# Performance work log

Measured on AMD Instinct MI355X. Metric: run time of the kernel, lower is better.

## Reference

```python
import jax, jax.numpy as jnp
import numpy as np

D_MODEL, N_HEADS, D_LLM = 1024, 16, 4096
D_KEYS = D_MODEL // N_HEADS  # 64


def setup_inputs() -> dict:
    key = jax.random.key(0)
    ks = jax.random.split(key, 11)
    s = lambda fan_in: 1.0 / np.sqrt(fan_in)
    inp = {
        "target_embedding": jax.random.normal(ks[0], (4, 2048, D_MODEL), jnp.float32),
        "source_embedding": jax.random.normal(ks[1], (4, 1024, D_LLM), jnp.float32),
        "value_embedding": jax.random.normal(ks[2], (4, 1024, D_LLM), jnp.float32),
        "Wq": jax.random.uniform(ks[3], (D_MODEL, D_KEYS * N_HEADS), jnp.float32, -s(D_MODEL), s(D_MODEL)),
        "bq": jax.random.uniform(ks[4], (D_KEYS * N_HEADS,), jnp.float32, -s(D_MODEL), s(D_MODEL)),
        "Wk": jax.random.uniform(ks[5], (D_LLM, D_KEYS * N_HEADS), jnp.float32, -s(D_LLM), s(D_LLM)),
        "bk": jax.random.uniform(ks[6], (D_KEYS * N_HEADS,), jnp.float32, -s(D_LLM), s(D_LLM)),
        "Wv": jax.random.uniform(ks[7], (D_LLM, D_KEYS * N_HEADS), jnp.float32, -s(D_LLM), s(D_LLM)),
        "bv": jax.random.uniform(ks[8], (D_KEYS * N_HEADS,), jnp.float32, -s(D_LLM), s(D_LLM)),
        "Wo": jax.random.uniform(ks[9], (D_KEYS * N_HEADS, D_MODEL), jnp.float32, -s(D_KEYS * N_HEADS), s(D_KEYS * N_HEADS)),
        "bo": jax.random.uniform(ks[10], (D_MODEL,), jnp.float32, -s(D_KEYS * N_HEADS), s(D_KEYS * N_HEADS)),
    }
    return inp


def reference(target_embedding, source_embedding, value_embedding,
              Wq, bq, Wk, bk, Wv, bv, Wo, bo):
    B, L, _ = target_embedding.shape
    _, S, _ = source_embedding.shape
    H, E = N_HEADS, D_KEYS
    q = (target_embedding @ Wq + bq).reshape(B, L, H, E)
    k = (source_embedding @ Wk + bk).reshape(B, S, H, E)
    v = (value_embedding @ Wv + bv).reshape(B, S, H, E)
    scale = 1.0 / np.sqrt(E)
    scores = jnp.einsum('blhe,bshe->bhls', q, k)  # [B,H,L,S]
    A = jax.nn.softmax(scale * scores, axis=-1)   # dropout = identity (eval mode)
    out = jnp.einsum('bhls,bshe->blhe', A, v).reshape(B, L, H * E)
    return out @ Wo + bo
```

## Files before the change

### kernel.cpp

```cpp
#include <hip/hip_runtime.h>
#include <hip/hip_bf16.h>

using bf16 = __hip_bfloat16;
typedef __attribute__((ext_vector_type(8))) short short8;
typedef __attribute__((ext_vector_type(4))) float f32x4;

static constexpr int Bc = 4, Lc = 2048, Sc = 1024;
static constexpr int DModel = 1024;

__device__ __forceinline__ void gload16(const void* g, void* l) {
  __builtin_amdgcn_global_load_lds((const __attribute__((address_space(1))) void*)g,
                                   (__attribute__((address_space(3))) void*)l,
                                   16, 0, 0);
}

__device__ __forceinline__ void wait_vm8()  { asm volatile("s_waitcnt vmcnt(8)" ::: "memory"); }
__device__ __forceinline__ void wait_vm6()  { asm volatile("s_waitcnt vmcnt(6)" ::: "memory"); }
__device__ __forceinline__ void wait_vm4()  { asm volatile("s_waitcnt vmcnt(4)" ::: "memory"); }
__device__ __forceinline__ void wait_vm3()  { asm volatile("s_waitcnt vmcnt(3)" ::: "memory"); }
__device__ __forceinline__ void wait_vm0()  { asm volatile("s_waitcnt vmcnt(0)" ::: "memory"); }
__device__ __forceinline__ void barrier_raw() { asm volatile("s_barrier" ::: "memory"); }

__global__ void cvt3(const float* __restrict__ a, bf16* __restrict__ ao, long na4,
                     const float* __restrict__ b, bf16* __restrict__ bo, long nb4,
                     const float* __restrict__ c, bf16* __restrict__ co, long nc4) {
  long total = na4 + nb4 + nc4;
  long stride = (long)gridDim.x * blockDim.x;
  for (long i = (long)blockIdx.x * blockDim.x + threadIdx.x; i < total; i += stride) {
    const float* src; bf16* dst; long j;
    if (i < na4)            { src = a; dst = ao; j = i; }
    else if (i < na4 + nb4) { src = b; dst = bo; j = i - na4; }
    else                    { src = c; dst = co; j = i - na4 - nb4; }
    float4 v = reinterpret_cast<const float4*>(src)[j];
    alignas(8) bf16 t[4] = {__float2bfloat16(v.x), __float2bfloat16(v.y),
                            __float2bfloat16(v.z), __float2bfloat16(v.w)};
    reinterpret_cast<ushort4*>(dst)[j] = *reinterpret_cast<const ushort4*>(t);
  }
}

__global__ __launch_bounds__(256) void transpose_cvt_w(const float* __restrict__ Wq, bf16* __restrict__ WqT,
                                                       const float* __restrict__ Wk, bf16* __restrict__ WkT,
                                                       const float* __restrict__ Wv, bf16* __restrict__ WvT,
                                                       const float* __restrict__ Wo, bf16* __restrict__ WoT) {
  __shared__ bf16 tile[32][33];
  int bid = blockIdx.x;
  const float* in; bf16* out; int R, l;
  if (bid < 1024)      { in = Wq; out = WqT; R = 1024; l = bid; }
  else if (bid < 5120) { in = Wk; out = WkT; R = 4096; l = bid - 1024; }
  else if (bid < 9216) { in = Wv; out = WvT; R = 4096; l = bid - 5120; }
  else                 { in = Wo; out = WoT; R = 1024; l = bid - 9216; }
  const int C = 1024;
  int bx = l & 31, by = l >> 5;
  int tx = threadIdx.x & 31, ty = threadIdx.x >> 5;
  int r0 = by * 32, c0 = bx * 32;
#pragma unroll
  for (int i = 0; i < 32; i += 8)
    tile[ty + i][tx] = __float2bfloat16(in[(long)(r0 + ty + i) * C + c0 + tx]);
  __syncthreads();
#pragma unroll
  for (int i = 0; i < 32; i += 8)
    out[(long)(c0 + ty + i) * R + r0 + tx] = tile[tx][ty + i];
}

__device__ __forceinline__ void gemm_bal_core(const bf16* __restrict__ A, const bf16* __restrict__ Bt,
                                              const float* __restrict__ bias,
                                              bf16* __restrict__ Cb, bf16* __restrict__ Cvt,
                                              int K, int bx, int by, bf16* lds) {
  const int tid = threadIdx.x;
  const int lane = tid & 63, g = lane >> 4, lm = lane & 15;
  const int wid = tid >> 6, wr = wid >> 1, wc = wid & 1;
  const long brow = (long)by * 256, bcol = (long)bx * 128;

  char* L = (char*)lds;
  const int rowA = tid >> 2;
  const int kg = (tid & 3) ^ ((rowA >> 1) & 3);
  const bf16* aS = A + (brow + rowA) * (long)K + kg * 8;
  const bf16* bS = Bt + (bcol + rowA) * (long)K + kg * 8;
  const long aOff1 = 128l * K;
  const int dA = tid * 16;

#define STAGEB(t_) {                                                     \
    const int _b = (t_) % 3; const long _ko = (long)(t_) * 32;           \
    gload16(aS + _ko,         L + _b * 24576 + dA);                      \
    gload16(aS + aOff1 + _ko, L + _b * 24576 + 8192 + dA);               \
    gload16(bS + _ko,         L + _b * 24576 + 16384 + dA); }

  f32x4 zero = {0.f, 0.f, 0.f, 0.f};
  f32x4 acc[4][4];
#pragma unroll
  for (int i = 0; i < 4; ++i)
#pragma unroll
    for (int j = 0; j < 4; ++j) acc[i][j] = zero;

  STAGEB(0);
  STAGEB(1);

  const int nt = K >> 5;
  for (int t = 0; t < nt; ++t) {
    if (t + 2 < nt)       { STAGEB(t + 2); wait_vm6(); }
    else if (t + 2 == nt) wait_vm3();
    else                  wait_vm0();
    barrier_raw();

    const char* Bf = L + (t % 3) * 24576;
    short8 aR[4], bR[4];
#pragma unroll
    for (int mi = 0; mi < 4; ++mi) {
      const int r = wr * 64 + mi * 16 + lm;
      aR[mi] = *reinterpret_cast<const short8*>(
          Bf + r * 64 + ((g ^ ((r >> 1) & 3)) << 4));
    }
#pragma unroll
    for (int ni = 0; ni < 4; ++ni) {
      const int r = wc * 64 + ni * 16 + lm;
      bR[ni] = *reinterpret_cast<const short8*>(
          Bf + 16384 + r * 64 + ((g ^ ((r >> 1) & 3)) << 4));
    }
    __builtin_amdgcn_s_setprio(1);
#pragma unroll
    for (int mi = 0; mi < 4; ++mi)
#pragma unroll
      for (int ni = 0; ni < 4; ++ni)
        acc[mi][ni] = __builtin_amdgcn_mfma_f32_16x16x32_bf16(aR[mi], bR[ni], acc[mi][ni], 0, 0, 0);
    __builtin_amdgcn_s_setprio(0);
    barrier_raw();
  }
#undef STAGEB

#pragma unroll
  for (int ni = 0; ni < 4; ++ni) {
    long n = bcol + wc * 64 + ni * 16 + lm;
    float bv = bias ? bias[n] : 0.f;
#pragma unroll
    for (int mi = 0; mi < 4; ++mi) {
      long m0 = brow + wr * 64 + mi * 16 + g * 4;
      if (Cvt) {
        long b = m0 >> 10, s0 = m0 & 1023;
        alignas(8) bf16 t4[4];
#pragma unroll
        for (int r = 0; r < 4; ++r) t4[r] = __float2bfloat16(acc[mi][ni][r] + bv);
        *reinterpret_cast<ushort4*>(Cvt + ((b << 10) + n) * 1024 + s0) =
            *reinterpret_cast<const ushort4*>(t4);
      } else {
#pragma unroll
        for (int r = 0; r < 4; ++r)
          Cb[(m0 + r) * 1024 + n] = __float2bfloat16(acc[mi][ni][r] + bv);
      }
    }
  }
}

__global__ __launch_bounds__(512, 4) void gemm_qkv_bal(
    const bf16* __restrict__ Ak, const bf16* __restrict__ Bk, const float* __restrict__ bk_, bf16* __restrict__ Ck, int Kk, int nbk,
    const bf16* __restrict__ Av, const bf16* __restrict__ Bv_, const float* __restrict__ bv_, bf16* __restrict__ CvT, int Kv, int nbv,
    const bf16* __restrict__ Aq, const bf16* __restrict__ Bq_, const float* __restrict__ bq_, bf16* __restrict__ Cq, int Kq) {
  __shared__ bf16 lds[36864];
  int bid = blockIdx.x;
  const bf16 *A, *Bt; const float* bias; bf16 *C = nullptr, *Cvt = nullptr; int K, l, nb;
  if (bid < nbk)            { A = Ak; Bt = Bk;  bias = bk_; C = Ck;    K = Kk; l = bid;             nb = nbk; }
  else if (bid < nbk + nbv) { A = Av; Bt = Bv_; bias = bv_; Cvt = CvT; K = Kv; l = bid - nbk;       nb = nbv; }
  else                      { A = Aq; Bt = Bq_; bias = bq_; C = Cq;   K = Kq; l = bid - nbk - nbv; nb = gridDim.x - nbk - nbv; }
  int g = (l & 7) * (nb >> 3) + (l >> 3);
  gemm_bal_core(A, Bt, bias, C, Cvt, K, g & 7, g >> 3, lds);
}

__device__ __forceinline__ void gemm_core(const bf16* __restrict__ A, const bf16* __restrict__ Bt,
                                          const float* __restrict__ bias,
                                          bf16* __restrict__ Cb, float* __restrict__ Cf,
                                          int N, int K, int bx, int by,
                                          bf16* As, bf16* Bs) {
  const int tid = threadIdx.x;
  const int lane = tid & 63, g = lane >> 4, lm = lane & 15;
  const int wid = tid >> 6, wr = wid >> 1, wc = wid & 1;
  const long brow = (long)by * 128, bcol = (long)bx * 128;

  const bf16* asrc[4];
  const bf16* bsrc[4];
  int dsto[4];
#pragma unroll
  for (int t = 0; t < 4; ++t) {
    int sl = tid + t * 256;
    int row = sl >> 3;
    int kg = (sl & 7) ^ (row & 7);
    asrc[t] = A + (brow + row) * (long)K + kg * 8;
    bsrc[t] = Bt + (bcol + row) * (long)K + kg * 8;
    dsto[t] = sl * 16;
  }

  f32x4 zero = {0.f, 0.f, 0.f, 0.f};
  f32x4 acc[4][4];
#pragma unroll
  for (int i = 0; i < 4; ++i)
#pragma unroll
    for (int j = 0; j < 4; ++j) acc[i][j] = zero;

  char* Asc = (char*)As;
  char* Bsc = (char*)Bs;

#pragma unroll
  for (int t = 0; t < 4; ++t) {
    gload16(asrc[t], Asc + dsto[t]);
    gload16(bsrc[t], Bsc + dsto[t]);
    asrc[t] += 64; bsrc[t] += 64;
  }

  const int nt = K >> 6;
  for (int i = 0; i < nt; ++i) {
    const int cur = i & 1;
    if (i + 1 < nt) {
      const int nxt = cur ^ 1;
#pragma unroll
      for (int t = 0; t < 4; ++t) {
        gload16(asrc[t], Asc + nxt * 16384 + dsto[t]);
        gload16(bsrc[t], Bsc + nxt * 16384 + dsto[t]);
        asrc[t] += 64; bsrc[t] += 64;
      }
      wait_vm8();
    } else {
      wait_vm0();
    }
    barrier_raw();

    const char* Ab = Asc + cur * 16384;
    const char* Bb = Bsc + cur * 16384;
    __builtin_amdgcn_s_setprio(1);
#pragma unroll
    for (int ks = 0; ks < 2; ++ks) {
      short8 af[4], bfv[4];
#pragma unroll
      for (int mi = 0; mi < 4; ++mi) {
        int m = wr * 64 + mi * 16 + lm;
        af[mi] = *reinterpret_cast<const short8*>(
            Ab + ((m * 128 + ks * 64 + g * 16) ^ ((m & 7) << 4)));
      }
#pragma unroll
      for (int ni = 0; ni < 4; ++ni) {
        int n = wc * 64 + ni * 16 + lm;
        bfv[ni] = *reinterpret_cast<const short8*>(
            Bb + ((n * 128 + ks * 64 + g * 16) ^ ((n & 7) << 4)));
      }
#pragma unroll
      for (int mi = 0; mi < 4; ++mi)
#pragma unroll
        for (int ni = 0; ni < 4; ++ni)
          acc[mi][ni] = __builtin_amdgcn_mfma_f32_16x16x32_bf16(af[mi], bfv[ni], acc[mi][ni], 0, 0, 0);
    }
    __builtin_amdgcn_s_setprio(0);
    barrier_raw();
  }

#pragma unroll
  for (int ni = 0; ni < 4; ++ni) {
    long n = bcol + wc * 64 + ni * 16 + lm;
    float bv = bias ? bias[n] : 0.f;
#pragma unroll
    for (int mi = 0; mi < 4; ++mi) {
      long m0 = brow + wr * 64 + mi * 16 + g * 4;
#pragma unroll
      for (int r = 0; r < 4; ++r) {
        float o = acc[mi][ni][r] + bv;
        if (Cb) Cb[(m0 + r) * N + n] = __float2bfloat16(o);
        else    Cf[(m0 + r) * N + n] = o;
      }
    }
  }
}

__global__ __launch_bounds__(256) void gemm_bt(const bf16* __restrict__ A,
                                               const bf16* __restrict__ Bt,
                                               const float* __restrict__ bias,
                                               bf16* __restrict__ Cb,
                                               float* __restrict__ Cf,
                                               int N, int K) {
  __shared__ bf16 As[2 * 128 * 64];
  __shared__ bf16 Bs[2 * 128 * 64];
  int bid = blockIdx.x;
  int g = (bid & 7) * (gridDim.x >> 3) + (bid >> 3);
  gemm_core(A, Bt, bias, Cb, Cf, N, K, g & 7, g >> 3, As, Bs);
}

__global__ __launch_bounds__(256) void attn_fused(const bf16* __restrict__ q,
                                                  const bf16* __restrict__ k,
                                                  const bf16* __restrict__ vT,
                                                  bf16* __restrict__ o) {
  constexpr float C2 = 0.18033688011112042f;
  constexpr float THR = 6.0f;
  __shared__ bf16 Kl[2][64 * 64];
  __shared__ bf16 Vl[2][64 * 64];
  __shared__ bf16 Pl[4][16 * 64];
  const int tid = threadIdx.x;
  const int lane = tid & 63, g = lane >> 4, lm = lane & 15;
  const int wid = tid >> 6;
  int bid = blockIdx.x;
  int gl = (bid & 7) * 256 + (bid >> 3);
  const int qt = gl & 31, bh = gl >> 5;
  const int b = bh >> 4, h = bh & 15;
  const int qbase = qt * 64 + wid * 16;

  const bf16* qrow = q + (long)(b * Lc + qbase + lm) * DModel + h * 64;
  short8 qa0 = *reinterpret_cast<const short8*>(qrow + g * 8);
  short8 qa1 = *reinterpret_cast<const short8*>(qrow + 32 + g * 8);
#pragma unroll
  for (int j = 0; j < 8; ++j) {
    union { ushort u; bf16 h; } cv;
    cv.u = (ushort)qa0[j];
    bf16 s0 = __float2bfloat16(__bfloat162float(cv.h) * C2);
    qa0[j] = (short)*reinterpret_cast<ushort*>(&s0);
    cv.u = (ushort)qa1[j];
    bf16 s1 = __float2bfloat16(__bfloat162float(cv.h) * C2);
    qa1[j] = (short)*reinterpret_cast<ushort*>(&s1);
  }

  const bf16* kbase = k + (long)b * Sc * DModel + h * 64;
  const bf16* vbase = vT + ((long)b * DModel + h * 64) * Sc;

  const bf16* ksrc[2];
  const bf16* vsrc[2];
  int dsto[2];
#pragma unroll
  for (int t = 0; t < 2; ++t) {
    int sl = tid + t * 256;
    int row = sl >> 3;
    int cg = (sl & 7) ^ (row & 7);
    ksrc[t] = kbase + (long)row * DModel + cg * 8;
    vsrc[t] = vbase + (long)row * Sc + cg * 8;
    dsto[t] = sl * 16;
  }

  f32x4 zero = {0.f, 0.f, 0.f, 0.f};
  f32x4 accO[4];
#pragma unroll
  for (int i = 0; i < 4; ++i) accO[i] = zero;
  f32x4 accL = zero;
  float mst[4] = {-1e30f, -1e30f, -1e30f, -1e30f};

  short8 vones;
#pragma unroll
  for (int j = 0; j < 8; ++j) vones[j] = (short)0x3F80;

  char* Klc = (char*)Kl;
  char* Vlc = (char*)Vl;
  char* Plc = (char*)Pl + wid * (16 * 64 * 2);

#pragma unroll
  for (int t = 0; t < 2; ++t) {
    gload16(ksrc[t], Klc + dsto[t]);
    gload16(vsrc[t], Vlc + dsto[t]);
    ksrc[t] += 64 * DModel; vsrc[t] += 64;
  }

  for (int j = 0; j < Sc / 64; ++j) {
    const int cur = j & 1;
    if (j + 1 < Sc / 64) {
      const int nxt = cur ^ 1;
#pragma unroll
      for (int t = 0; t < 2; ++t) {
        gload16(ksrc[t], Klc + nxt * 8192 + dsto[t]);
        gload16(vsrc[t], Vlc + nxt * 8192 + dsto[t]);
        ksrc[t] += 64 * DModel; vsrc[t] += 64;
      }
      wait_vm4();
    } else {
      wait_vm0();
    }
    barrier_raw();

    const char* Kb = Klc + cur * 8192;
    const char* Vb = Vlc + cur * 8192;

    f32x4 scv[4];
    __builtin_amdgcn_s_setprio(1);
#pragma unroll
    for (int st = 0; st < 4; ++st) {
      int s = st * 16 + lm;
      int sw = (s & 7) << 4;
      short8 kb0 = *reinterpret_cast<const short8*>(Kb + ((s * 128 + g * 16) ^ sw));
      short8 kb1 = *reinterpret_cast<const short8*>(Kb + ((s * 128 + 64 + g * 16) ^ sw));
      f32x4 z = zero;
      z = __builtin_amdgcn_mfma_f32_16x16x32_bf16(qa0, kb0, z, 0, 0, 0);
      z = __builtin_amdgcn_mfma_f32_16x16x32_bf16(qa1, kb1, z, 0, 0, 0);
      scv[st] = z;
    }
    __builtin_amdgcn_s_setprio(0);

    float pmax[4];
#pragma unroll
    for (int r = 0; r < 4; ++r)
      pmax[r] = fmaxf(fmaxf(scv[0][r], scv[1][r]), fmaxf(scv[2][r], scv[3][r]));
    int need = 0;
#pragma unroll
    for (int r = 0; r < 4; ++r) need |= (pmax[r] > mst[r] + THR) ? 1 : 0;
    if (__any(need)) {
#pragma unroll
      for (int r = 0; r < 4; ++r) {
        float mx = pmax[r];
        mx = fmaxf(mx, __shfl_xor(mx, 1));
        mx = fmaxf(mx, __shfl_xor(mx, 2));
        mx = fmaxf(mx, __shfl_xor(mx, 4));
        mx = fmaxf(mx, __shfl_xor(mx, 8));
        float mnew = fmaxf(mst[r], mx);
        float corr = __builtin_amdgcn_exp2f(mst[r] - mnew);
        mst[r] = mnew;
        accL[r] *= corr;
#pragma unroll
        for (int et = 0; et < 4; ++et) accO[et][r] *= corr;
      }
    }
#pragma unroll
    for (int r = 0; r < 4; ++r) {
      int qq = g * 4 + r;
      int swp = (qq & 7) << 4;
#pragma unroll
      for (int st = 0; st < 4; ++st) {
        float p = __builtin_amdgcn_exp2f(scv[st][r] - mst[r]);
        *reinterpret_cast<bf16*>(Plc + ((qq * 128 + (st * 16 + lm) * 2) ^ swp)) =
            __float2bfloat16(p);
      }
    }

    __builtin_amdgcn_s_setprio(1);
#pragma unroll
    for (int sk = 0; sk < 2; ++sk) {
      short8 pa = *reinterpret_cast<const short8*>(
          Plc + ((lm * 128 + sk * 64 + g * 16) ^ ((lm & 7) << 4)));
      accL = __builtin_amdgcn_mfma_f32_16x16x32_bf16(pa, vones, accL, 0, 0, 0);
#pragma unroll
      for (int et = 0; et < 4; ++et) {
        int e = et * 16 + lm;
        short8 vb = *reinterpret_cast<const short8*>(
            Vb + ((e * 128 + sk * 64 + g * 16) ^ ((e & 7) << 4)));
        accO[et] = __builtin_amdgcn_mfma_f32_16x16x32_bf16(pa, vb, accO[et], 0, 0, 0);
      }
    }
    __builtin_amdgcn_s_setprio(0);
    barrier_raw();
  }

#pragma unroll
  for (int r = 0; r < 4; ++r) {
    float inv = 1.0f / accL[r];
    long row = (long)(b * Lc + qbase + g * 4 + r);
#pragma unroll
    for (int et = 0; et < 4; ++et)
      o[row * DModel + h * 64 + et * 16 + lm] = __float2bfloat16(accO[et][r] * inv);
  }
}

extern "C" void kernel_launch(void* const* d_in, const int* in_sizes, int n_in,
                              void* d_out, int out_size, void* d_ws, size_t ws_size,
                              hipStream_t stream) {
  const float* tgt = (const float*)d_in[0];
  const float* src = (const float*)d_in[1];
  const float* val = (const float*)d_in[2];
  const float* Wq  = (const float*)d_in[3];
  const float* bq  = (const float*)d_in[4];
  const float* Wk  = (const float*)d_in[5];
  const float* bk  = (const float*)d_in[6];
  const float* Wv  = (const float*)d_in[7];
  const float* bv  = (const float*)d_in[8];
  const float* Wo  = (const float*)d_in[9];
  const float* bo  = (const float*)d_in[10];
  float* out = (float*)d_out;
  char* ws = (char*)d_ws;

  const long n4_tgt = (long)8192 * 1024 / 4;
  const long n4_sv  = (long)4096 * 4096 / 4;

  if (ws_size < (132ul << 20)) return;

  bf16* WqT  = (bf16*)(ws + (0l   << 20));
  bf16* WkT  = (bf16*)(ws + (2l   << 20));
  bf16* WvT  = (bf16*)(ws + (10l  << 20));
  bf16* WoT  = (bf16*)(ws + (18l  << 20));
  bf16* tgtb = (bf16*)(ws + (20l  << 20));
  bf16* srcb = (bf16*)(ws + (36l  << 20));
  bf16* valb = (bf16*)(ws + (68l  << 20));
  bf16* qb   = (bf16*)(ws + (100l << 20));
  bf16* kb   = (bf16*)(ws + (116l << 20));
  bf16* vTb  = (bf16*)(ws + (124l << 20));
  bf16* attnb = tgtb;

  transpose_cvt_w<<<10240, 256, 0, stream>>>(Wq, WqT, Wk, WkT, Wv, WvT, Wo, WoT);
  cvt3<<<4096, 256, 0, stream>>>(tgt, tgtb, n4_tgt, src, srcb, n4_sv, val, valb, n4_sv);
  gemm_qkv_bal<<<512, 512, 0, stream>>>(srcb, WkT, bk, kb, 4096, 128,
                                        valb, WvT, bv, vTb, 4096, 128,
                                        tgtb, WqT, bq, qb, 1024);
  attn_fused<<<2048, 256, 0, stream>>>(qb, kb, vTb, attnb);
  gemm_bt<<<512, 256, 0, stream>>>(attnb, WoT, bo, (bf16*)nullptr, out, 1024, 1024);
}
```

Before: 242.8 us.

## Fuse fp32-to-bf16 activation conversion into QKV GEMM A-operand loading

Removes the separate cvt3 pass that converted the target, source and value embeddings to bf16. The QKV GEMM now loads fp32 A tiles straight into registers, converts them, and writes bf16 to LDS, while B still uses direct global-to-LDS loads. The loop is unrolled by two with even and odd register sets to keep loads overlapped. This drops a full extra read and write of roughly 160MB of activations, but doubles the A-operand global traffic inside the GEMM and adds conversion ALU work and LDS stores on the main loop.

```diff
diff --git a/kernel.cpp b/kernel.cpp
--- a/kernel.cpp
+++ b/kernel.cpp
@@ -16,26 +16,16 @@
 
 __device__ __forceinline__ void wait_vm8()  { asm volatile("s_waitcnt vmcnt(8)" ::: "memory"); }
 __device__ __forceinline__ void wait_vm6()  { asm volatile("s_waitcnt vmcnt(6)" ::: "memory"); }
+__device__ __forceinline__ void wait_vm5()  { asm volatile("s_waitcnt vmcnt(5)" ::: "memory"); }
 __device__ __forceinline__ void wait_vm4()  { asm volatile("s_waitcnt vmcnt(4)" ::: "memory"); }
-__device__ __forceinline__ void wait_vm3()  { asm volatile("s_waitcnt vmcnt(3)" ::: "memory"); }
+__device__ __forceinline__ void wait_vm1()  { asm volatile("s_waitcnt vmcnt(1)" ::: "memory"); }
 __device__ __forceinline__ void wait_vm0()  { asm volatile("s_waitcnt vmcnt(0)" ::: "memory"); }
+__device__ __forceinline__ void lgkm0()     { asm volatile("s_waitcnt lgkmcnt(0)" ::: "memory"); }
 __device__ __forceinline__ void barrier_raw() { asm volatile("s_barrier" ::: "memory"); }
 
-__global__ void cvt3(const float* __restrict__ a, bf16* __restrict__ ao, long na4,
-                     const float* __restrict__ b, bf16* __restrict__ bo, long nb4,
-                     const float* __restrict__ c, bf16* __restrict__ co, long nc4) {
-  long total = na4 + nb4 + nc4;
-  long stride = (long)gridDim.x * blockDim.x;
-  for (long i = (long)blockIdx.x * blockDim.x + threadIdx.x; i < total; i += stride) {
-    const float* src; bf16* dst; long j;
-    if (i < na4)            { src = a; dst = ao; j = i; }
-    else if (i < na4 + nb4) { src = b; dst = bo; j = i - na4; }
-    else                    { src = c; dst = co; j = i - na4 - nb4; }
-    float4 v = reinterpret_cast<const float4*>(src)[j];
-    alignas(8) bf16 t[4] = {__float2bfloat16(v.x), __float2bfloat16(v.y),
-                            __float2bfloat16(v.z), __float2bfloat16(v.w)};
-    reinterpret_cast<ushort4*>(dst)[j] = *reinterpret_cast<const ushort4*>(t);
-  }
+__device__ __forceinline__ short b2s(float f) {
+  bf16 h = __float2bfloat16(f);
+  return (short)*reinterpret_cast<ushort*>(&h);
 }
 
 __global__ __launch_bounds__(256) void transpose_cvt_w(const float* __restrict__ Wq, bf16* __restrict__ WqT,
@@ -62,7 +52,7 @@
     out[(long)(c0 + ty + i) * R + r0 + tx] = tile[tx][ty + i];
 }
 
-__device__ __forceinline__ void gemm_bal_core(const bf16* __restrict__ A, const bf16* __restrict__ Bt,
+__device__ __forceinline__ void gemm_bal_core(const float* __restrict__ Af, const bf16* __restrict__ Bt,
                                               const float* __restrict__ bias,
                                               bf16* __restrict__ Cb, bf16* __restrict__ Cvt,
                                               int K, int bx, int by, bf16* lds) {
@@ -72,18 +62,53 @@
   const long brow = (long)by * 256, bcol = (long)bx * 128;
 
   char* L = (char*)lds;
-  const int rowA = tid >> 2;
-  const int kg = (tid & 3) ^ ((rowA >> 1) & 3);
-  const bf16* aS = A + (brow + rowA) * (long)K + kg * 8;
-  const bf16* bS = Bt + (bcol + rowA) * (long)K + kg * 8;
-  const long aOff1 = 128l * K;
-  const int dA = tid * 16;
-
-#define STAGEB(t_) {                                                     \
-    const int _b = (t_) % 3; const long _ko = (long)(t_) * 32;           \
-    gload16(aS + _ko,         L + _b * 24576 + dA);                      \
-    gload16(aS + aOff1 + _ko, L + _b * 24576 + 8192 + dA);               \
-    gload16(bS + _ko,         L + _b * 24576 + 16384 + dA); }
+
+  const int rowB = tid >> 2;
+  const int kgB = (tid & 3) ^ ((rowB >> 1) & 3);
+  const bf16* bS = Bt + (bcol + rowB) * (long)K + kgB * 8;
+  const int dB = tid * 16;
+
+  const int rA = tid >> 1, kh = tid & 1;
+  const float* aS = Af + (brow + rA) * (long)K + kh * 16;
+  const int swzA = (rA >> 1) & 3;
+  const int dA0 = rA * 64 + ((((kh << 1) | 0) ^ swzA) << 4);
+  const int dA1 = rA * 64 + ((((kh << 1) | 1) ^ swzA) << 4);
+
+#define ISSUE_A(t_, V0, V1, V2, V3) {                                          \
+    const float4* _ap = reinterpret_cast<const float4*>(aS + (long)(t_) * 32); \
+    V0 = _ap[0]; V1 = _ap[1]; V2 = _ap[2]; V3 = _ap[3]; }
+#define ISSUE_B(t_) gload16(bS + (long)(t_) * 32, L + ((t_) % 3) * 24576 + 16384 + dB);
+#define DSW_A(t_, V0, V1, V2, V3) {                                            \
+    char* _d = L + ((t_) % 3) * 24576;                                         \
+    short8 _w0 = { b2s(V0.x), b2s(V0.y), b2s(V0.z), b2s(V0.w),                 \
+                   b2s(V1.x), b2s(V1.y), b2s(V1.z), b2s(V1.w) };               \
+    short8 _w1 = { b2s(V2.x), b2s(V2.y), b2s(V2.z), b2s(V2.w),                 \
+                   b2s(V3.x), b2s(V3.y), b2s(V3.z), b2s(V3.w) };               \
+    *reinterpret_cast<short8*>(_d + dA0) = _w0;                                \
+    *reinterpret_cast<short8*>(_d + dA1) = _w1; }
+#define COMPUTE(t_) {                                                          \
+    const char* Bf = L + ((t_) % 3) * 24576;                                   \
+    short8 aR[4], bR[4];                                                       \
+    _Pragma("unroll")                                                          \
+    for (int mi = 0; mi < 4; ++mi) {                                           \
+      const int r_ = wr * 64 + mi * 16 + lm;                                   \
+      aR[mi] = *reinterpret_cast<const short8*>(                               \
+          Bf + r_ * 64 + ((g ^ ((r_ >> 1) & 3)) << 4));                        \
+    }                                                                          \
+    _Pragma("unroll")                                                          \
+    for (int ni = 0; ni < 4; ++ni) {                                           \
+      const int r_ = wc * 64 + ni * 16 + lm;                                   \
+      bR[ni] = *reinterpret_cast<const short8*>(                               \
+          Bf + 16384 + r_ * 64 + ((g ^ ((r_ >> 1) & 3)) << 4));                \
+    }                                                                          \
+    __builtin_amdgcn_s_setprio(1);                                             \
+    _Pragma("unroll")                                                          \
+    for (int mi = 0; mi < 4; ++mi)                                             \
+      _Pragma("unroll")                                                        \
+      for (int ni = 0; ni < 4; ++ni)                                           \
+        acc[mi][ni] = __builtin_amdgcn_mfma_f32_16x16x32_bf16(                 \
+            aR[mi], bR[ni], acc[mi][ni], 0, 0, 0);                             \
+    __builtin_amdgcn_s_setprio(0); }
 
   f32x4 zero = {0.f, 0.f, 0.f, 0.f};
   f32x4 acc[4][4];
@@ -92,40 +117,39 @@
 #pragma unroll
     for (int j = 0; j < 4; ++j) acc[i][j] = zero;
 
-  STAGEB(0);
-  STAGEB(1);
+  float4 e0, e1, e2, e3, o0, o1, o2, o3;
+
+  ISSUE_A(0, e0, e1, e2, e3); ISSUE_B(0);
+  ISSUE_A(1, o0, o1, o2, o3); ISSUE_B(1);
+  wait_vm6();
+  DSW_A(0, e0, e1, e2, e3);
+  wait_vm5();
 
   const int nt = K >> 5;
-  for (int t = 0; t < nt; ++t) {
-    if (t + 2 < nt)       { STAGEB(t + 2); wait_vm6(); }
-    else if (t + 2 == nt) wait_vm3();
-    else                  wait_vm0();
+  for (int tt = 0; tt < nt; tt += 2) {
+    if (tt + 2 < nt)       { ISSUE_A(tt + 2, e0, e1, e2, e3); ISSUE_B(tt + 2); wait_vm6(); }
+    else if (tt + 2 == nt) { wait_vm1(); }
+    else                   { wait_vm0(); }
+    if (tt + 1 < nt) DSW_A(tt + 1, o0, o1, o2, o3);
+    lgkm0();
     barrier_raw();
-
-    const char* Bf = L + (t % 3) * 24576;
-    short8 aR[4], bR[4];
-#pragma unroll
-    for (int mi = 0; mi < 4; ++mi) {
-      const int r = wr * 64 + mi * 16 + lm;
-      aR[mi] = *reinterpret_cast<const short8*>(
-          Bf + r * 64 + ((g ^ ((r >> 1) & 3)) << 4));
-    }
-#pragma unroll
-    for (int ni = 0; ni < 4; ++ni) {
-      const int r = wc * 64 + ni * 16 + lm;
-      bR[ni] = *reinterpret_cast<const short8*>(
-          Bf + 16384 + r * 64 + ((g ^ ((r >> 1) & 3)) << 4));
-    }
-    __builtin_amdgcn_s_setprio(1);
-#pragma unroll
-    for (int mi = 0; mi < 4; ++mi)
-#pragma unroll
-      for (int ni = 0; ni < 4; ++ni)
-        acc[mi][ni] = __builtin_amdgcn_mfma_f32_16x16x32_bf16(aR[mi], bR[ni], acc[mi][ni], 0, 0, 0);
-    __builtin_amdgcn_s_setprio(0);
+    COMPUTE(tt);
     barrier_raw();
-  }
-#undef STAGEB
+    if (tt + 1 < nt) {
+      if (tt + 3 < nt)       { ISSUE_A(tt + 3, o0, o1, o2, o3); ISSUE_B(tt + 3); wait_vm6(); }
+      else if (tt + 3 == nt) { wait_vm1(); }
+      else                   { wait_vm0(); }
+      if (tt + 2 < nt) DSW_A(tt + 2, e0, e1, e2, e3);
+      lgkm0();
+      barrier_raw();
+      COMPUTE(tt + 1);
+      barrier_raw();
+    }
+  }
+#undef ISSUE_A
+#undef ISSUE_B
+#undef DSW_A
+#undef COMPUTE
 
 #pragma unroll
   for (int ni = 0; ni < 4; ++ni) {
@@ -151,12 +175,12 @@
 }
 
 __global__ __launch_bounds__(512, 4) void gemm_qkv_bal(
-    const bf16* __restrict__ Ak, const bf16* __restrict__ Bk, const float* __restrict__ bk_, bf16* __restrict__ Ck, int Kk, int nbk,
-    const bf16* __restrict__ Av, const bf16* __restrict__ Bv_, const float* __restrict__ bv_, bf16* __restrict__ CvT, int Kv, int nbv,
-    const bf16* __restrict__ Aq, const bf16* __restrict__ Bq_, const float* __restrict__ bq_, bf16* __restrict__ Cq, int Kq) {
+    const float* __restrict__ Ak, const bf16* __restrict__ Bk, const float* __restrict__ bk_, bf16* __restrict__ Ck, int Kk, int nbk,
+    const float* __restrict__ Av, const bf16* __restrict__ Bv_, const float* __restrict__ bv_, bf16* __restrict__ CvT, int Kv, int nbv,
+    const float* __restrict__ Aq, const bf16* __restrict__ Bq_, const float* __restrict__ bq_, bf16* __restrict__ Cq, int Kq) {
   __shared__ bf16 lds[36864];
   int bid = blockIdx.x;
-  const bf16 *A, *Bt; const float* bias; bf16 *C = nullptr, *Cvt = nullptr; int K, l, nb;
+  const float* A; const bf16* Bt; const float* bias; bf16 *C = nullptr, *Cvt = nullptr; int K, l, nb;
   if (bid < nbk)            { A = Ak; Bt = Bk;  bias = bk_; C = Ck;    K = Kk; l = bid;             nb = nbk; }
   else if (bid < nbk + nbv) { A = Av; Bt = Bv_; bias = bv_; Cvt = CvT; K = Kv; l = bid - nbk;       nb = nbv; }
   else                      { A = Aq; Bt = Bq_; bias = bq_; C = Cq;   K = Kq; l = bid - nbk - nbv; nb = gridDim.x - nbk - nbv; }
@@ -463,28 +487,21 @@
   float* out = (float*)d_out;
   char* ws = (char*)d_ws;
 
-  const long n4_tgt = (long)8192 * 1024 / 4;
-  const long n4_sv  = (long)4096 * 4096 / 4;
-
-  if (ws_size < (132ul << 20)) return;
-
-  bf16* WqT  = (bf16*)(ws + (0l   << 20));
-  bf16* WkT  = (bf16*)(ws + (2l   << 20));
-  bf16* WvT  = (bf16*)(ws + (10l  << 20));
-  bf16* WoT  = (bf16*)(ws + (18l  << 20));
-  bf16* tgtb = (bf16*)(ws + (20l  << 20));
-  bf16* srcb = (bf16*)(ws + (36l  << 20));
-  bf16* valb = (bf16*)(ws + (68l  << 20));
-  bf16* qb   = (bf16*)(ws + (100l << 20));
-  bf16* kb   = (bf16*)(ws + (116l << 20));
-  bf16* vTb  = (bf16*)(ws + (124l << 20));
-  bf16* attnb = tgtb;
+  if (ws_size < (68ul << 20)) return;
+
+  bf16* WqT   = (bf16*)(ws + (0l  << 20));
+  bf16* WkT   = (bf16*)(ws + (2l  << 20));
+  bf16* WvT   = (bf16*)(ws + (10l << 20));
+  bf16* WoT   = (bf16*)(ws + (18l << 20));
+  bf16* attnb = (bf16*)(ws + (20l << 20));
+  bf16* qb    = (bf16*)(ws + (36l << 20));
+  bf16* kb    = (bf16*)(ws + (52l << 20));
+  bf16* vTb   = (bf16*)(ws + (60l << 20));
 
   transpose_cvt_w<<<10240, 256, 0, stream>>>(Wq, WqT, Wk, WkT, Wv, WvT, Wo, WoT);
-  cvt3<<<4096, 256, 0, stream>>>(tgt, tgtb, n4_tgt, src, srcb, n4_sv, val, valb, n4_sv);
-  gemm_qkv_bal<<<512, 512, 0, stream>>>(srcb, WkT, bk, kb, 4096, 128,
-                                        valb, WvT, bv, vTb, 4096, 128,
-                                        tgtb, WqT, bq, qb, 1024);
+  gemm_qkv_bal<<<512, 512, 0, stream>>>(src, WkT, bk, kb, 4096, 128,
+                                        val, WvT, bv, vTb, 4096, 128,
+                                        tgt, WqT, bq, qb, 1024);
   attn_fused<<<2048, 256, 0, stream>>>(qb, kb, vTb, attnb);
   gemm_bt<<<512, 256, 0, stream>>>(attnb, WoT, bo, (bf16*)nullptr, out, 1024, 1024);
 }
```

After: 457.5 us. +88.5%, slower.

## Merge weight/input conversion kernels and double attention query tile per block

Applied to the files above, without the earlier changes.

The two preprocessing kernels (weight transpose-convert and activation convert) become one launch, with blocks split by index, which saves a kernel launch and lets the two jobs overlap. The attention kernel now uses 512 threads (8 waves) per block covering 128 query rows instead of 64. Each K/V tile loaded into LDS is shared by twice as many waves, halving the number of K/V loads per thread and the total K/V traffic. The trade-off is fewer blocks (1024), bigger blocks, and more waves waiting at each barrier.

```diff
diff --git a/kernel.cpp b/kernel.cpp
--- a/kernel.cpp
+++ b/kernel.cpp
@@ -16,50 +16,53 @@
 
 __device__ __forceinline__ void wait_vm8()  { asm volatile("s_waitcnt vmcnt(8)" ::: "memory"); }
 __device__ __forceinline__ void wait_vm6()  { asm volatile("s_waitcnt vmcnt(6)" ::: "memory"); }
-__device__ __forceinline__ void wait_vm4()  { asm volatile("s_waitcnt vmcnt(4)" ::: "memory"); }
 __device__ __forceinline__ void wait_vm3()  { asm volatile("s_waitcnt vmcnt(3)" ::: "memory"); }
+__device__ __forceinline__ void wait_vm2()  { asm volatile("s_waitcnt vmcnt(2)" ::: "memory"); }
 __device__ __forceinline__ void wait_vm0()  { asm volatile("s_waitcnt vmcnt(0)" ::: "memory"); }
 __device__ __forceinline__ void barrier_raw() { asm volatile("s_barrier" ::: "memory"); }
 
-__global__ void cvt3(const float* __restrict__ a, bf16* __restrict__ ao, long na4,
-                     const float* __restrict__ b, bf16* __restrict__ bo, long nb4,
-                     const float* __restrict__ c, bf16* __restrict__ co, long nc4) {
-  long total = na4 + nb4 + nc4;
-  long stride = (long)gridDim.x * blockDim.x;
-  for (long i = (long)blockIdx.x * blockDim.x + threadIdx.x; i < total; i += stride) {
-    const float* src; bf16* dst; long j;
-    if (i < na4)            { src = a; dst = ao; j = i; }
-    else if (i < na4 + nb4) { src = b; dst = bo; j = i - na4; }
-    else                    { src = c; dst = co; j = i - na4 - nb4; }
-    float4 v = reinterpret_cast<const float4*>(src)[j];
-    alignas(8) bf16 t[4] = {__float2bfloat16(v.x), __float2bfloat16(v.y),
-                            __float2bfloat16(v.z), __float2bfloat16(v.w)};
-    reinterpret_cast<ushort4*>(dst)[j] = *reinterpret_cast<const ushort4*>(t);
-  }
-}
-
-__global__ __launch_bounds__(256) void transpose_cvt_w(const float* __restrict__ Wq, bf16* __restrict__ WqT,
-                                                       const float* __restrict__ Wk, bf16* __restrict__ WkT,
-                                                       const float* __restrict__ Wv, bf16* __restrict__ WvT,
-                                                       const float* __restrict__ Wo, bf16* __restrict__ WoT) {
+__global__ __launch_bounds__(256) void prep(
+    const float* __restrict__ Wq, bf16* __restrict__ WqT,
+    const float* __restrict__ Wk, bf16* __restrict__ WkT,
+    const float* __restrict__ Wv, bf16* __restrict__ WvT,
+    const float* __restrict__ Wo, bf16* __restrict__ WoT,
+    const float* __restrict__ a, bf16* __restrict__ ao, long na4,
+    const float* __restrict__ b, bf16* __restrict__ bo, long nb4,
+    const float* __restrict__ c, bf16* __restrict__ co, long nc4) {
   __shared__ bf16 tile[32][33];
   int bid = blockIdx.x;
-  const float* in; bf16* out; int R, l;
-  if (bid < 1024)      { in = Wq; out = WqT; R = 1024; l = bid; }
-  else if (bid < 5120) { in = Wk; out = WkT; R = 4096; l = bid - 1024; }
-  else if (bid < 9216) { in = Wv; out = WvT; R = 4096; l = bid - 5120; }
-  else                 { in = Wo; out = WoT; R = 1024; l = bid - 9216; }
-  const int C = 1024;
-  int bx = l & 31, by = l >> 5;
-  int tx = threadIdx.x & 31, ty = threadIdx.x >> 5;
-  int r0 = by * 32, c0 = bx * 32;
-#pragma unroll
-  for (int i = 0; i < 32; i += 8)
-    tile[ty + i][tx] = __float2bfloat16(in[(long)(r0 + ty + i) * C + c0 + tx]);
-  __syncthreads();
-#pragma unroll
-  for (int i = 0; i < 32; i += 8)
-    out[(long)(c0 + ty + i) * R + r0 + tx] = tile[tx][ty + i];
+  if (bid < 10240) {
+    const float* in; bf16* out; int R, l;
+    if (bid < 1024)      { in = Wq; out = WqT; R = 1024; l = bid; }
+    else if (bid < 5120) { in = Wk; out = WkT; R = 4096; l = bid - 1024; }
+    else if (bid < 9216) { in = Wv; out = WvT; R = 4096; l = bid - 5120; }
+    else                 { in = Wo; out = WoT; R = 1024; l = bid - 9216; }
+    const int C = 1024;
+    int bx = l & 31, by = l >> 5;
+    int tx = threadIdx.x & 31, ty = threadIdx.x >> 5;
+    int r0 = by * 32, c0 = bx * 32;
+#pragma unroll
+    for (int i = 0; i < 32; i += 8)
+      tile[ty + i][tx] = __float2bfloat16(in[(long)(r0 + ty + i) * C + c0 + tx]);
+    __syncthreads();
+#pragma unroll
+    for (int i = 0; i < 32; i += 8)
+      out[(long)(c0 + ty + i) * R + r0 + tx] = tile[tx][ty + i];
+  } else {
+    int cb = bid - 10240;
+    long total = na4 + nb4 + nc4;
+    long stride = (long)(gridDim.x - 10240) * blockDim.x;
+    for (long i = (long)cb * blockDim.x + threadIdx.x; i < total; i += stride) {
+      const float* src; bf16* dst; long j;
+      if (i < na4)            { src = a; dst = ao; j = i; }
+      else if (i < na4 + nb4) { src = b; dst = bo; j = i - na4; }
+      else                    { src = c; dst = co; j = i - na4 - nb4; }
+      float4 v = reinterpret_cast<const float4*>(src)[j];
+      alignas(8) bf16 t[4] = {__float2bfloat16(v.x), __float2bfloat16(v.y),
+                              __float2bfloat16(v.z), __float2bfloat16(v.w)};
+      reinterpret_cast<ushort4*>(dst)[j] = *reinterpret_cast<const ushort4*>(t);
+    }
+  }
 }
 
 __device__ __forceinline__ void gemm_bal_core(const bf16* __restrict__ A, const bf16* __restrict__ Bt,
@@ -279,7 +282,7 @@
   gemm_core(A, Bt, bias, Cb, Cf, N, K, g & 7, g >> 3, As, Bs);
 }
 
-__global__ __launch_bounds__(256) void attn_fused(const bf16* __restrict__ q,
+__global__ __launch_bounds__(512) void attn_fused(const bf16* __restrict__ q,
                                                   const bf16* __restrict__ k,
                                                   const bf16* __restrict__ vT,
                                                   bf16* __restrict__ o) {
@@ -287,15 +290,15 @@
   constexpr float THR = 6.0f;
   __shared__ bf16 Kl[2][64 * 64];
   __shared__ bf16 Vl[2][64 * 64];
-  __shared__ bf16 Pl[4][16 * 64];
+  __shared__ bf16 Pl[8][16 * 64];
   const int tid = threadIdx.x;
   const int lane = tid & 63, g = lane >> 4, lm = lane & 15;
   const int wid = tid >> 6;
   int bid = blockIdx.x;
-  int gl = (bid & 7) * 256 + (bid >> 3);
-  const int qt = gl & 31, bh = gl >> 5;
+  int gl = (bid & 7) * 128 + (bid >> 3);
+  const int qt = gl & 15, bh = gl >> 4;
   const int b = bh >> 4, h = bh & 15;
-  const int qbase = qt * 64 + wid * 16;
+  const int qbase = qt * 128 + wid * 16;
 
   const bf16* qrow = q + (long)(b * Lc + qbase + lm) * DModel + h * 64;
   short8 qa0 = *reinterpret_cast<const short8*>(qrow + g * 8);
@@ -314,18 +317,11 @@
   const bf16* kbase = k + (long)b * Sc * DModel + h * 64;
   const bf16* vbase = vT + ((long)b * DModel + h * 64) * Sc;
 
-  const bf16* ksrc[2];
-  const bf16* vsrc[2];
-  int dsto[2];
-#pragma unroll
-  for (int t = 0; t < 2; ++t) {
-    int sl = tid + t * 256;
-    int row = sl >> 3;
-    int cg = (sl & 7) ^ (row & 7);
-    ksrc[t] = kbase + (long)row * DModel + cg * 8;
-    vsrc[t] = vbase + (long)row * Sc + cg * 8;
-    dsto[t] = sl * 16;
-  }
+  const int srow = tid >> 3;
+  const int scg = (tid & 7) ^ (srow & 7);
+  const bf16* ksrc = kbase + (long)srow * DModel + scg * 8;
+  const bf16* vsrc = vbase + (long)srow * Sc + scg * 8;
+  const int dsto = tid * 16;
 
   f32x4 zero = {0.f, 0.f, 0.f, 0.f};
   f32x4 accO[4];
@@ -342,24 +338,18 @@
   char* Vlc = (char*)Vl;
   char* Plc = (char*)Pl + wid * (16 * 64 * 2);
 
-#pragma unroll
-  for (int t = 0; t < 2; ++t) {
-    gload16(ksrc[t], Klc + dsto[t]);
-    gload16(vsrc[t], Vlc + dsto[t]);
-    ksrc[t] += 64 * DModel; vsrc[t] += 64;
-  }
+  gload16(ksrc, Klc + dsto);
+  gload16(vsrc, Vlc + dsto);
+  ksrc += 64 * DModel; vsrc += 64;
 
   for (int j = 0; j < Sc / 64; ++j) {
     const int cur = j & 1;
     if (j + 1 < Sc / 64) {
       const int nxt = cur ^ 1;
-#pragma unroll
-      for (int t = 0; t < 2; ++t) {
-        gload16(ksrc[t], Klc + nxt * 8192 + dsto[t]);
-        gload16(vsrc[t], Vlc + nxt * 8192 + dsto[t]);
-        ksrc[t] += 64 * DModel; vsrc[t] += 64;
-      }
-      wait_vm4();
+      gload16(ksrc, Klc + nxt * 8192 + dsto);
+      gload16(vsrc, Vlc + nxt * 8192 + dsto);
+      ksrc += 64 * DModel; vsrc += 64;
+      wait_vm2();
     } else {
       wait_vm0();
     }
@@ -480,11 +470,12 @@
   bf16* vTb  = (bf16*)(ws + (124l << 20));
   bf16* attnb = tgtb;
 
-  transpose_cvt_w<<<10240, 256, 0, stream>>>(Wq, WqT, Wk, WkT, Wv, WvT, Wo, WoT);
-  cvt3<<<4096, 256, 0, stream>>>(tgt, tgtb, n4_tgt, src, srcb, n4_sv, val, valb, n4_sv);
+  prep<<<10240 + 4096, 256, 0, stream>>>(Wq, WqT, Wk, WkT, Wv, WvT, Wo, WoT,
+                                         tgt, tgtb, n4_tgt, src, srcb, n4_sv,
+                                         val, valb, n4_sv);
   gemm_qkv_bal<<<512, 512, 0, stream>>>(srcb, WkT, bk, kb, 4096, 128,
                                         valb, WvT, bv, vTb, 4096, 128,
                                         tgtb, WqT, bq, qb, 1024);
-  attn_fused<<<2048, 256, 0, stream>>>(qb, kb, vTb, attnb);
+  attn_fused<<<1024, 512, 0, stream>>>(qb, kb, vTb, attnb);
   gemm_bt<<<512, 256, 0, stream>>>(attnb, WoT, bo, (bf16*)nullptr, out, 1024, 1024);
 }
```

After: 227.9 us. 6.1% less time.
